# Kernel tuning notes

Measured on AMD Instinct MI355X. Metric: run time of the kernel, lower is better.

The kernel has to match this reference:

```python
import jax, jax.numpy as jnp
import numpy as np

N = 6000      # nodes
E = 150000    # edges (avg degree ~25, close to _AVG_DEGREE=23.4)
K = 9         # (lmax+1)^2 spherical coefficients, lmax=2
C = 128       # sphere_channels
H = 8         # num_heads
V = 16        # attn_value_channels (H*V == C)
L = 2         # num_layers
B = 512       # num_distance_basis
RMAX = 5.0
EPS = 1e-6


def _rms_sh(x):
    # rms_norm_sh-style normalization over (coefficients, channels)
    return x * jax.lax.rsqrt(jnp.mean(x * x, axis=(-2, -1), keepdims=True) + EPS)


def _seg_softmax(logits, seg, n):
    # numerically-stable per-destination-node softmax over incoming edges
    m = jax.ops.segment_max(logits, seg, num_segments=n)
    ex = jnp.exp(logits - m[seg])
    s = jax.ops.segment_sum(ex, seg, num_segments=n)
    return ex / (s[seg] + 1e-9)


def setup_inputs() -> dict:
    key = jax.random.key(0)
    ks = jax.random.split(key, 24)
    s = 0.02
    inp = {
        # graph / features
        "atom_feats": jax.random.randint(ks[0], (N, 4), 0, 10),
        "bond_feats": jax.random.randint(ks[1], (E, 3), 0, 8),
        "edge_index": jax.random.randint(ks[2], (2, E), 0, N),
        "edge_distance": jax.random.uniform(ks[3], (E,), jnp.float32, 0.0, RMAX),
        # embeddings
        "atom_emb": jax.random.normal(ks[4], (4, 10, C), jnp.float32) * s,
        "bond_emb": jax.random.normal(ks[5], (3, 8, C), jnp.float32) * s,
        # distance-basis edge MLP (edge_channels_list = [512, 128, 128])
        "W_rbf1": jax.random.normal(ks[6], (B, C), jnp.float32) * s,
        "b_rbf1": jnp.zeros((C,), jnp.float32),
        "W_rbf2": jax.random.normal(ks[7], (C, C), jnp.float32) * s,
        "b_rbf2": jnp.zeros((C,), jnp.float32),
        # per-layer attention params (stacked over L)
        "Wa1": jax.random.normal(ks[8], (L, 3 * C, C), jnp.float32) * s,
        "Wa2": jax.random.normal(ks[9], (L, C, H), jnp.float32) * s,
        "Wv": jax.random.normal(ks[10], (L, C, H * V), jnp.float32) * s,
        "Wg": jax.random.normal(ks[11], (L, C, H), jnp.float32) * s,
        "Wo": jax.random.normal(ks[12], (L, H * V, C), jnp.float32) * s,
        # per-layer FFN params
        "Wf1": jax.random.normal(ks[13], (L, C, 512), jnp.float32) * s,
        "Wf2": jax.random.normal(ks[14], (L, 512, C), jnp.float32) * s,
    }
    return inp


def _forward(atom_feats, bond_feats, edge_index, edge_distance,
             atom_emb, bond_emb, W_rbf1, b_rbf1, W_rbf2, b_rbf2,
             Wa1, Wa2, Wv, Wg, Wo, Wf1, Wf2):
    src, dst = edge_index[0], edge_index[1]

    # --- atom embedding into l=0 coefficient of the SH node state ---
    a0 = sum(atom_emb[f][atom_feats[:, f]] for f in range(4))      # [N, C]
    x = jnp.zeros((N, K, C), a0.dtype).at[:, 0, :].set(a0)          # [N, K, C]

    # --- gaussian distance basis + edge embedding MLP + bond features ---
    centers = jnp.linspace(0.0, RMAX, B)
    width = RMAX / B
    rbf = jnp.exp(-((edge_distance[:, None] - centers[None, :]) / width) ** 2)  # [E, B]
    e = jax.nn.silu(rbf @ W_rbf1 + b_rbf1) @ W_rbf2 + b_rbf2                    # [E, C]
    e = e + sum(bond_emb[f][bond_feats[:, f]] for f in range(3))

    for l in range(L):
        # ---- SO(2)-style graph attention block ----
        xn = _rms_sh(x)
        xs = xn[src]                                                 # [E, K, C] gather
        inv = jnp.concatenate([xn[src, 0], xn[dst, 0], e], axis=-1)  # invariant feats [E, 3C]
        logits = jax.nn.silu(inv @ Wa1[l]) @ Wa2[l]                  # [E, H]
        alpha = _seg_softmax(logits, dst, N)                         # renormalized attention
        gate = jax.nn.sigmoid(e @ Wg[l])                             # edge-embedding gate [E, H]
        v = jnp.einsum('ekc,chv->ekhv', xs, Wv[l].reshape(C, H, V))  # [E, K, H, V]
        v = v * (alpha * gate)[:, None, :, None]
        msg = v.reshape(E, K, H * V)
        agg = jax.ops.segment_sum(msg, dst, num_segments=N)          # scatter [N, K, H*V]
        x = x + jnp.einsum('nkd,dc->nkc', agg, Wo[l])

        # ---- equivariant FFN with separable S2-style activation ----
        xn = _rms_sh(x)
        h = jnp.einsum('nkc,cf->nkf', xn, Wf1[l])                    # [N, K, 512]
        h0 = jax.nn.silu(h[:, :1, :])                                # l=0 scalar path
        hr = h[:, 1:, :] * jax.nn.sigmoid(h[:, :1, :])               # gated l>0 path
        h = jnp.concatenate([h0, hr], axis=1)
        x = x + jnp.einsum('nkf,fc->nkc', h, Wf2[l])

    return _rms_sh(x)


def reference(atom_feats, bond_feats, edge_index, edge_distance,
              atom_emb, bond_emb, W_rbf1, b_rbf1, W_rbf2, b_rbf2,
              Wa1, Wa2, Wv, Wg, Wo, Wf1, Wf2):
    return _forward(atom_feats, bond_feats, edge_index, edge_distance,
                    atom_emb, bond_emb, W_rbf1, b_rbf1, W_rbf2, b_rbf2,
                    Wa1, Wa2, Wv, Wg, Wo, Wf1, Wf2)
```

## Files before the change

### kernel.cpp

```cpp
#include <hip/hip_runtime.h>

#define NN 6000
#define NE 150000
#define TBM 2048
#define TROWS (TBM + 1)

typedef unsigned int uint;
typedef unsigned short ushort;
typedef __attribute__((ext_vector_type(8))) short short8v;
typedef __attribute__((ext_vector_type(4))) float float4v;

__device__ __forceinline__ float siluf(float x) { return x / (1.f + __expf(-x)); }
__device__ __forceinline__ float sigmf(float x) { return 1.f / (1.f + __expf(-x)); }
__device__ __forceinline__ uint pack2bf(float lo, float hi) {
    uint ul = __float_as_uint(lo);
    ul = (ul + 0x7fffu + ((ul >> 16) & 1u)) >> 16;
    uint uh = __float_as_uint(hi);
    uh = ((uh + 0x7fffu + ((uh >> 16) & 1u)) >> 16) << 16;
    return ul | uh;
}
__device__ __forceinline__ ushort f2bf(float f) {
    uint u = __float_as_uint(f);
    return (ushort)((u + 0x7fffu + ((u >> 16) & 1u)) >> 16);
}
__device__ __forceinline__ float2 up2(uint u) {
    return make_float2(__uint_as_float(u << 16), __uint_as_float(u & 0xffff0000u));
}

__global__ __launch_bounds__(256)
void k_prep(const float* __restrict__ W2, const float* __restrict__ b2,
            const float* __restrict__ Wa1, const float* __restrict__ Wg,
            const float* __restrict__ bemb,
            const float* __restrict__ Wf1, const float* __restrict__ Wf2,
            const float* __restrict__ Wv, const float* __restrict__ Wa2,
            const float* __restrict__ Wo,
            float* __restrict__ W2A, float* __restrict__ W2G,
            float* __restrict__ bA, float* __restrict__ bG,
            uint* __restrict__ BAcb, float* __restrict__ BGc,
            ushort* __restrict__ Wf1x, ushort* __restrict__ Wf2x,
            ushort* __restrict__ Wvx, ushort* __restrict__ Wa1sx,
            ushort* __restrict__ Wa1dx, ushort* __restrict__ Wa2x,
            ushort* __restrict__ Wox)
{
    __shared__ float w2_s[8][132];
    const int l = blockIdx.y, bx = blockIdx.x, tid = threadIdx.x;
    const float* Wa1e = Wa1 + (size_t)l * 384 * 128 + 256 * 128;
    const float* Wgl  = Wg  + (size_t)l * 128 * 8;

    if (bx < 16) {
        const int i0 = bx * 8;
        for (int q = tid; q < 8 * 32; q += 256) {
            int ni = q >> 5, j4 = (q & 31) * 4;
            *reinterpret_cast<float4*>(&w2_s[ni][j4]) =
                *reinterpret_cast<const float4*>(&W2[(size_t)(i0 + ni) * 128 + j4]);
        }
        __syncthreads();
        const int j = tid & 127, ng = tid >> 7;
        float a[4] = {0.f, 0.f, 0.f, 0.f};
        #pragma unroll 4
        for (int k4 = 0; k4 < 128; k4 += 4) {
            float w0 = Wa1e[(k4 + 0) * 128 + j];
            float w1 = Wa1e[(k4 + 1) * 128 + j];
            float w2v = Wa1e[(k4 + 2) * 128 + j];
            float w3 = Wa1e[(k4 + 3) * 128 + j];
            #pragma unroll
            for (int r = 0; r < 4; ++r) {
                const float4 xv = *reinterpret_cast<const float4*>(&w2_s[ng * 4 + r][k4]);
                a[r] += xv.x * w0 + xv.y * w1 + xv.z * w2v + xv.w * w3;
            }
        }
        #pragma unroll
        for (int r = 0; r < 4; ++r)
            W2A[(size_t)l * 16384 + (size_t)(i0 + ng * 4 + r) * 128 + j] = a[r];
    } else if (bx == 16) {
        const int i = tid & 127, hq = tid >> 7;
        float a[4] = {0.f, 0.f, 0.f, 0.f};
        for (int k = 0; k < 128; ++k) {
            float w = W2[(size_t)i * 128 + k];
            const float4 g4 = *reinterpret_cast<const float4*>(&Wgl[k * 8 + hq * 4]);
            a[0] += w * g4.x; a[1] += w * g4.y; a[2] += w * g4.z; a[3] += w * g4.w;
        }
        #pragma unroll
        for (int q = 0; q < 4; ++q)
            W2G[(size_t)l * 1024 + (size_t)i * 8 + hq * 4 + q] = a[q];
    } else if (bx == 17) {
        if (tid < 128) {
            float s = 0.f;
            for (int k = 0; k < 128; ++k) s += b2[k] * Wa1e[k * 128 + tid];
            bA[l * 128 + tid] = s;
        } else if (tid < 136) {
            int h = tid - 128;
            float s = 0.f;
            for (int k = 0; k < 128; ++k) s += b2[k] * Wgl[k * 8 + h];
            bG[l * 8 + h] = s;
        }
    } else if (bx < 274) {
        const int cb = (bx - 18) * 2 + (tid >> 7);
        const int c = tid & 127;
        const int b[3] = {cb >> 6, (cb >> 3) & 7, cb & 7};
        float s = 0.f;
        #pragma unroll
        for (int f = 0; f < 3; ++f) {
            const float* er = &bemb[(size_t)(f * 8 + b[f]) * 128];
            for (int k = 0; k < 128; ++k)
                s += er[k] * Wa1e[k * 128 + c];
        }
        float hi = __shfl_down(s, 1, 64);
        if ((c & 1) == 0)
            BAcb[(size_t)l * 512 * 64 + (size_t)cb * 64 + (c >> 1)] = pack2bf(s, hi);
        if (c < 8) {
            float g = 0.f;
            #pragma unroll
            for (int f = 0; f < 3; ++f) {
                const float* er = &bemb[(size_t)(f * 8 + b[f]) * 128];
                for (int k = 0; k < 128; ++k)
                    g += er[k] * Wgl[k * 8 + c];
            }
            BGc[(size_t)l * 512 * 8 + (size_t)cb * 8 + c] = g;
        }
    } else {
        const int sub = (bx - 274) * 4 + (tid >> 6);
        const int lane = tid & 63;
        if (sub < 128) {
            const int nt = sub >> 2, kt = sub & 3;
            const float* src = Wf1 + (size_t)l * 65536;
            ushort* dst = Wf1x + (size_t)l * 65536 + ((size_t)sub * 64 + lane) * 8;
            #pragma unroll
            for (int j = 0; j < 8; ++j)
                dst[j] = f2bf(src[(size_t)(kt * 32 + (lane >> 4) * 8 + j) * 512 + nt * 16 + (lane & 15)]);
        } else if (sub < 256) {
            const int b2x = sub - 128;
            const int nt = b2x >> 4, kt = b2x & 15;
            const float* src = Wf2 + (size_t)l * 65536;
            ushort* dst = Wf2x + (size_t)l * 65536 + ((size_t)b2x * 64 + lane) * 8;
            #pragma unroll
            for (int j = 0; j < 8; ++j)
                dst[j] = f2bf(src[(size_t)(kt * 32 + (lane >> 4) * 8 + j) * 128 + nt * 16 + (lane & 15)]);
        } else if (sub < 352) {
            const int b3 = sub - 256;
            const int mat = b3 >> 5, blk = b3 & 31;
            const int nt = blk >> 2, kt = blk & 3;
            const float* src;
            ushort* dst;
            if (mat == 0)      { src = Wv  + (size_t)l * 16384;             dst = Wvx   + (size_t)l * 16384; }
            else if (mat == 1) { src = Wa1 + (size_t)l * 384 * 128;         dst = Wa1sx + (size_t)l * 16384; }
            else               { src = Wa1 + (size_t)l * 384 * 128 + 16384; dst = Wa1dx + (size_t)l * 16384; }
            dst += ((size_t)blk * 64 + lane) * 8;
            #pragma unroll
            for (int j = 0; j < 8; ++j)
                dst[j] = f2bf(src[(size_t)(kt * 32 + (lane >> 4) * 8 + j) * 128 + nt * 16 + (lane & 15)]);
        } else if (sub < 356) {
            const int kt = sub - 352;
            const int col = lane & 15;
            const float* src = Wa2 + (size_t)l * 128 * 8;
            ushort* dst = Wa2x + (size_t)l * 2048 + ((size_t)kt * 64 + lane) * 8;
            #pragma unroll
            for (int j = 0; j < 8; ++j) {
                int krow = kt * 32 + (lane >> 4) * 8 + j;
                dst[j] = (col < 8) ? f2bf(src[(size_t)krow * 8 + col]) : (ushort)0;
            }
        } else {
            const int blk = sub - 356;
            const int nt = blk >> 2, kt = blk & 3;
            const float* src = Wo + (size_t)l * 16384;
            ushort* dst = Wox + (size_t)l * 16384 + ((size_t)blk * 64 + lane) * 8;
            #pragma unroll
            for (int j = 0; j < 8; ++j)
                dst[j] = f2bf(src[(size_t)(kt * 32 + (lane >> 4) * 8 + j) * 128 + nt * 16 + (lane & 15)]);
        }
    }
}

__device__ __forceinline__
void node_gemm3(const ushort a_s[16][136], int tid, int n0,
                const ushort* __restrict__ Wvx, const ushort* __restrict__ Wa1sx,
                const ushort* __restrict__ Wa1dx,
                uint* __restrict__ Vb, uint* __restrict__ Psb, uint* __restrict__ Pdb)
{
    const int l = tid & 63, wq = tid >> 6;
    const int lr = l & 15, lk = l >> 4;
    #pragma unroll
    for (int jb = 0; jb < 6; ++jb) {
        int job = wq * 6 + jb;
        int mat = job >> 3, nt = job & 7;
        const ushort* W = (mat == 0) ? Wvx : (mat == 1 ? Wa1sx : Wa1dx);
        uint* O = (mat == 0) ? Vb : (mat == 1 ? Psb : Pdb);
        float4v acc = (float4v){0.f, 0.f, 0.f, 0.f};
        #pragma unroll
        for (int ks = 0; ks < 4; ++ks) {
            short8v af = *reinterpret_cast<const short8v*>(&a_s[lr][lk * 8 + ks * 32]);
            short8v bf = *reinterpret_cast<const short8v*>(&W[((size_t)(nt * 4 + ks) * 64 + l) * 8]);
            acc = __builtin_amdgcn_mfma_f32_16x16x32_bf16(af, bf, acc, 0, 0, 0);
        }
        #pragma unroll
        for (int r = 0; r < 4; ++r) {
            float v = acc[r];
            float vn = __shfl_xor(v, 1, 64);
            if ((l & 1) == 0) {
                int row = lk * 4 + r, col = nt * 16 + lr;
                O[(size_t)(n0 + row) * 64 + (col >> 1)] = pack2bf(v, vn);
            }
        }
    }
}

__global__ __launch_bounds__(256)
void k_prep2(const float* __restrict__ W1, const float* __restrict__ b1,
             const float* __restrict__ W2A, const float* __restrict__ W2G,
             const float* __restrict__ bA, const float* __restrict__ bG,
             uint* __restrict__ TAb, float* __restrict__ TG,
             const int* __restrict__ af, const float* __restrict__ aemb,
             float* __restrict__ x, int* __restrict__ deg,
             const ushort* __restrict__ Wvx, const ushort* __restrict__ Wa1sx,
             const ushort* __restrict__ Wa1dx,
             uint* __restrict__ Vb, uint* __restrict__ Psb, uint* __restrict__ Pdb)
{
    __shared__ float rbf_s[8][32];
    __shared__ int   bs_s[8];
    __shared__ float t1_s[8][132];
    __shared__ ushort a_s[16][136];
    const int tid = threadIdx.x, bx = blockIdx.x;

    if (bx < 514) {
        const int l = (bx >= 257) ? 1 : 0;
        const int r0 = (bx - l * 257) * 8;
        {
            int ri = tid >> 5, j = tid & 31;
            int row = min(r0 + ri, TBM);
            float d = (float)row * (5.0f / TBM);
            const float step = 5.0f / 511.0f;
            const float invw = 512.0f / 5.0f;
            int b0 = (int)(d * (511.0f / 5.0f) + 0.5f);
            int bs = min(max(b0 - 16, 0), 512 - 32);
            if (j == 0) bs_s[ri] = bs;
            float z = (d - (float)(bs + j) * step) * invw;
            rbf_s[ri][j] = __expf(-z * z);
        }
        __syncthreads();
        #pragma unroll
        for (int pass = 0; pass < 4; ++pass) {
            int idx = pass * 256 + tid;
            int ri = idx >> 7, c = idx & 127;
            int bs = bs_s[ri];
            float t = b1[c];
            #pragma unroll
            for (int j = 0; j < 32; ++j)
                t += rbf_s[ri][j] * W1[(bs + j) * 128 + c];
            t1_s[ri][c] = siluf(t);
        }
        __syncthreads();

        const float* W2Al = W2A + (size_t)l * 16384;
        const int c = tid & 127, ng = tid >> 7;
        float a[4];
        #pragma unroll
        for (int r = 0; r < 4; ++r) a[r] = bA[l * 128 + c];
        #pragma unroll 4
        for (int k4 = 0; k4 < 128; k4 += 4) {
            float w0 = W2Al[(k4 + 0) * 128 + c];
            float w1 = W2Al[(k4 + 1) * 128 + c];
            float w2v = W2Al[(k4 + 2) * 128 + c];
            float w3 = W2Al[(k4 + 3) * 128 + c];
            #pragma unroll
            for (int r = 0; r < 4; ++r) {
                const float4 xv = *reinterpret_cast<const float4*>(&t1_s[ng * 4 + r][k4]);
                a[r] += xv.x * w0 + xv.y * w1 + xv.z * w2v + xv.w * w3;
            }
        }
        #pragma unroll
        for (int r = 0; r < 4; ++r) {
            float hi = __shfl_down(a[r], 1, 64);
            int row = r0 + ng * 4 + r;
            if (((c & 1) == 0) && row <= TBM)
                TAb[(size_t)l * TROWS * 64 + (size_t)row * 64 + (c >> 1)] = pack2bf(a[r], hi);
        }
        if (tid < 64) {
            int ri = tid >> 3, h = tid & 7;
            int row = r0 + ri;
            if (row <= TBM) {
                const float* W2Gl = W2G + (size_t)l * 1024;
                float s = bG[l * 8 + h];
                #pragma unroll 8
                for (int k = 0; k < 128; ++k)
                    s += t1_s[ri][k] * W2Gl[k * 8 + h];
                TG[(size_t)l * TROWS * 8 + (size_t)row * 8 + h] = s;
            }
        }
    } else {
        const int n0 = (bx - 514) * 16;
        if (tid < 16) deg[n0 + tid] = 0;
        {
            int ni = tid >> 4, c8 = (tid & 15) * 8;
            int n = n0 + ni;
            float v[8];
            #pragma unroll
            for (int q = 0; q < 8; ++q) v[q] = 0.f;
            #pragma unroll
            for (int f = 0; f < 4; ++f) {
                int idx = af[n * 4 + f];
                const float* er = &aemb[(size_t)(f * 10 + idx) * 128 + c8];
                float4 e0 = *reinterpret_cast<const float4*>(er);
                float4 e1 = *reinterpret_cast<const float4*>(er + 4);
                v[0] += e0.x; v[1] += e0.y; v[2] += e0.z; v[3] += e0.w;
                v[4] += e1.x; v[5] += e1.y; v[6] += e1.z; v[7] += e1.w;
            }
            float* xr = &x[(size_t)n * 128 + c8];
            *reinterpret_cast<float4*>(xr)     = make_float4(v[0], v[1], v[2], v[3]);
            *reinterpret_cast<float4*>(xr + 4) = make_float4(v[4], v[5], v[6], v[7]);
            float ss = 0.f;
            #pragma unroll
            for (int q = 0; q < 8; ++q) ss += v[q] * v[q];
            #pragma unroll
            for (int m = 1; m < 16; m <<= 1) ss += __shfl_xor(ss, m, 16);
            float r = rsqrtf(ss * (1.0f / 1152.0f) + 1e-6f);
            uint4 pk;
            pk.x = pack2bf(v[0] * r, v[1] * r);
            pk.y = pack2bf(v[2] * r, v[3] * r);
            pk.z = pack2bf(v[4] * r, v[5] * r);
            pk.w = pack2bf(v[6] * r, v[7] * r);
            *reinterpret_cast<uint4*>(&a_s[ni][c8]) = pk;
        }
        __syncthreads();
        node_gemm3(a_s, tid, n0, Wvx, Wa1sx, Wa1dx, Vb, Psb, Pdb);
    }
}

__global__ __launch_bounds__(256)
void k_hist(const int* __restrict__ eidx, int* __restrict__ deg)
{
    int e = blockIdx.x * 256 + threadIdx.x;
    if (e < NE) atomicAdd(&deg[eidx[NE + e]], 1);
}

__global__ __launch_bounds__(1024)
void k_scan(const int* __restrict__ deg, int* __restrict__ off, int* __restrict__ cursor)
{
    __shared__ int part[1024];
    const int t = threadIdx.x;
    const int base = t * 6;
    int loc[6]; int s = 0;
    #pragma unroll
    for (int i = 0; i < 6; ++i) {
        int d = (base + i < NN) ? deg[base + i] : 0;
        loc[i] = s; s += d;
    }
    part[t] = s;
    __syncthreads();
    for (int o = 1; o < 1024; o <<= 1) {
        int v = (t >= o) ? part[t - o] : 0;
        __syncthreads();
        part[t] += v;
        __syncthreads();
    }
    int pre = (t > 0) ? part[t - 1] : 0;
    #pragma unroll
    for (int i = 0; i < 6; ++i) {
        if (base + i < NN) {
            int v = pre + loc[i];
            off[base + i] = v;
            cursor[base + i] = v;
        }
    }
    if (t == 1023) off[NN] = part[1023];
}

__global__ __launch_bounds__(256)
void k_fill(const int* __restrict__ eidx, const int* __restrict__ bondf,
            const float* __restrict__ dist, int* __restrict__ cursor,
            int* __restrict__ srcp, int* __restrict__ dstp,
            float* __restrict__ distp, int* __restrict__ cbp)
{
    int e = blockIdx.x * 256 + threadIdx.x;
    if (e < NE) {
        int d = eidx[NE + e];
        int p = atomicAdd(&cursor[d], 1);
        srcp[p] = eidx[e];
        dstp[p] = d;
        distp[p] = dist[e];
        cbp[p] = bondf[e * 3 + 0] * 64 + bondf[e * 3 + 1] * 8 + bondf[e * 3 + 2];
    }
}

__global__ __launch_bounds__(256)
void k_attn(const int* __restrict__ srcp, const int* __restrict__ dstp,
            const float* __restrict__ distp, const int* __restrict__ cbp,
            const uint* __restrict__ Psb, const uint* __restrict__ Pdb,
            const uint* __restrict__ TAbl, const float* __restrict__ TGl,
            const uint* __restrict__ BAcbl, const float* __restrict__ BGcl,
            const ushort* __restrict__ Wa2xl,
            float2* __restrict__ nex)
{
    __shared__ ushort t_s[32][136];
    __shared__ float gate_s[32][8];
    const int tid = threadIdx.x;
    const int p0 = blockIdx.x * 32;

    {
        const int ei = tid >> 3, g = tid & 7;
        const int p = min(p0 + ei, NE - 1);
        const int sn = srcp[p], dn = dstp[p];
        const float d = distp[p];
        const int cb = cbp[p];
        float u = d * ((float)TBM / 5.0f);
        int i = min((int)u, TBM - 1);
        float f = u - (float)i, f1 = 1.f - f;

        uint ps[8], pd[8], t0[8], t1v[8], ba[8];
        {
            const uint4* pp = reinterpret_cast<const uint4*>(&Psb[(size_t)sn * 64 + g * 8]);
            uint4 a = pp[0], b = pp[1];
            ps[0]=a.x; ps[1]=a.y; ps[2]=a.z; ps[3]=a.w; ps[4]=b.x; ps[5]=b.y; ps[6]=b.z; ps[7]=b.w;
            pp = reinterpret_cast<const uint4*>(&Pdb[(size_t)dn * 64 + g * 8]);
            a = pp[0]; b = pp[1];
            pd[0]=a.x; pd[1]=a.y; pd[2]=a.z; pd[3]=a.w; pd[4]=b.x; pd[5]=b.y; pd[6]=b.z; pd[7]=b.w;
            pp = reinterpret_cast<const uint4*>(&TAbl[(size_t)i * 64 + g * 8]);
            a = pp[0]; b = pp[1];
            t0[0]=a.x; t0[1]=a.y; t0[2]=a.z; t0[3]=a.w; t0[4]=b.x; t0[5]=b.y; t0[6]=b.z; t0[7]=b.w;
            pp = reinterpret_cast<const uint4*>(&TAbl[(size_t)(i + 1) * 64 + g * 8]);
            a = pp[0]; b = pp[1];
            t1v[0]=a.x; t1v[1]=a.y; t1v[2]=a.z; t1v[3]=a.w; t1v[4]=b.x; t1v[5]=b.y; t1v[6]=b.z; t1v[7]=b.w;
            pp = reinterpret_cast<const uint4*>(&BAcbl[(size_t)cb * 64 + g * 8]);
            a = pp[0]; b = pp[1];
            ba[0]=a.x; ba[1]=a.y; ba[2]=a.z; ba[3]=a.w; ba[4]=b.x; ba[5]=b.y; ba[6]=b.z; ba[7]=b.w;
        }
        uint tw[8];
        #pragma unroll
        for (int q = 0; q < 8; ++q) {
            float2 vs = up2(ps[q]), vd = up2(pd[q]), v0 = up2(t0[q]), v1 = up2(t1v[q]), vb = up2(ba[q]);
            float s0 = siluf(vs.x + vd.x + f1 * v0.x + f * v1.x + vb.x);
            float s1 = siluf(vs.y + vd.y + f1 * v0.y + f * v1.y + vb.y);
            tw[q] = pack2bf(s0, s1);
        }
        uint4* tp = reinterpret_cast<uint4*>(&t_s[ei][g * 16]);
        tp[0] = make_uint4(tw[0], tw[1], tw[2], tw[3]);
        tp[1] = make_uint4(tw[4], tw[5], tw[6], tw[7]);
        if (g == 0) {
            const float4* tg0 = reinterpret_cast<const float4*>(&TGl[(size_t)i * 8]);
            const float4* bg4 = reinterpret_cast<const float4*>(&BGcl[(size_t)cb * 8]);
            #pragma unroll
            for (int q = 0; q < 2; ++q) {
                float4 g0 = tg0[q], g1 = tg0[q + 2], bb = bg4[q];
                gate_s[ei][4 * q + 0] = f1 * g0.x + f * g1.x + bb.x;
                gate_s[ei][4 * q + 1] = f1 * g0.y + f * g1.y + bb.y;
                gate_s[ei][4 * q + 2] = f1 * g0.z + f * g1.z + bb.z;
                gate_s[ei][4 * q + 3] = f1 * g0.w + f * g1.w + bb.w;
            }
        }
    }
    __syncthreads();

    {
        const int wq = tid >> 6, l = tid & 63;
        if (wq < 2) {
            const int lr = l & 15, lk = l >> 4;
            float4v acc = (float4v){0.f, 0.f, 0.f, 0.f};
            #pragma unroll
            for (int ks = 0; ks < 4; ++ks) {
                short8v af = *reinterpret_cast<const short8v*>(&t_s[wq * 16 + lr][lk * 8 + ks * 32]);
                short8v bf = *reinterpret_cast<const short8v*>(&Wa2xl[((size_t)ks * 64 + l) * 8]);
                acc = __builtin_amdgcn_mfma_f32_16x16x32_bf16(af, bf, acc, 0, 0, 0);
            }
            const int h = l & 15;
            if (h < 8) {
                #pragma unroll
                for (int r = 0; r < 4; ++r) {
                    int ei = wq * 16 + lk * 4 + r;
                    int p = p0 + ei;
                    if (p < NE) {
                        float ex = __expf(acc[r]);
                        nex[(size_t)p * 8 + h] = make_float2(ex * sigmf(gate_s[ei][h]), ex);
                    }
                }
            }
        }
    }
}

template<int LAST>
__global__ __launch_bounds__(256)
void k_layer_fused(float* __restrict__ x,
                   const int* __restrict__ off, const int* __restrict__ srcp,
                   const float2* __restrict__ nex, const uint* __restrict__ Vb,
                   const ushort* __restrict__ Woxl,
                   const ushort* __restrict__ Wf1xl, const ushort* __restrict__ Wf2xl,
                   float* __restrict__ out,
                   const ushort* __restrict__ WvxN, const ushort* __restrict__ Wa1sxN,
                   const ushort* __restrict__ Wa1dxN,
                   uint* __restrict__ VbO, uint* __restrict__ Psb, uint* __restrict__ Pdb)
{
    __shared__ ushort a_s[16][136];
    __shared__ ushort h_s[16][520];
    __shared__ float xf_s[16][132];
    const int tid = threadIdx.x;
    const int n0 = blockIdx.x * 16;
    const int ni = tid >> 4, c8 = (tid & 15) * 8;

    {
        const float* xr = &x[(size_t)(n0 + ni) * 128 + c8];
        *reinterpret_cast<float4*>(&xf_s[ni][c8])     = *reinterpret_cast<const float4*>(xr);
        *reinterpret_cast<float4*>(&xf_s[ni][c8 + 4]) = *reinterpret_cast<const float4*>(xr + 4);
    }

    {
        const int n = n0 + ni;
        const int h = (tid & 15) >> 1;
        const int cd4 = (tid & 15) * 4;
        const int s = off[n], t = off[n + 1];
        float acc[8];
        #pragma unroll
        for (int q = 0; q < 8; ++q) acc[q] = 0.f;
        float es = 0.f;
        int p = s;
        for (; p + 4 <= t; p += 4) {
            int sn0 = srcp[p + 0], sn1 = srcp[p + 1], sn2 = srcp[p + 2], sn3 = srcp[p + 3];
            float2 ne0 = nex[(size_t)(p + 0) * 8 + h];
            float2 ne1 = nex[(size_t)(p + 1) * 8 + h];
            float2 ne2 = nex[(size_t)(p + 2) * 8 + h];
            float2 ne3 = nex[(size_t)(p + 3) * 8 + h];
            uint4 u0 = *reinterpret_cast<const uint4*>(&Vb[(size_t)sn0 * 64 + cd4]);
            uint4 u1 = *reinterpret_cast<const uint4*>(&Vb[(size_t)sn1 * 64 + cd4]);
            uint4 u2 = *reinterpret_cast<const uint4*>(&Vb[(size_t)sn2 * 64 + cd4]);
            uint4 u3 = *reinterpret_cast<const uint4*>(&Vb[(size_t)sn3 * 64 + cd4]);
            es += ne0.y + ne1.y + ne2.y + ne3.y;
            uint uu[4][4] = {{u0.x,u0.y,u0.z,u0.w},{u1.x,u1.y,u1.z,u1.w},
                             {u2.x,u2.y,u2.z,u2.w},{u3.x,u3.y,u3.z,u3.w}};
            float cf[4] = {ne0.x, ne1.x, ne2.x, ne3.x};
            #pragma unroll
            for (int e = 0; e < 4; ++e) {
                #pragma unroll
                for (int q = 0; q < 4; ++q) {
                    float2 v = up2(uu[e][q]);
                    acc[2 * q + 0] += cf[e] * v.x;
                    acc[2 * q + 1] += cf[e] * v.y;
                }
            }
        }
        for (; p < t; ++p) {
            int sn = srcp[p];
            float2 ne = nex[(size_t)p * 8 + h];
            uint4 u = *reinterpret_cast<const uint4*>(&Vb[(size_t)sn * 64 + cd4]);
            es += ne.y;
            uint uu[4] = {u.x, u.y, u.z, u.w};
            #pragma unroll
            for (int q = 0; q < 4; ++q) {
                float2 v = up2(uu[q]);
                acc[2 * q + 0] += ne.x * v.x;
                acc[2 * q + 1] += ne.x * v.y;
            }
        }
        float sinv = 1.f / (es + 1e-9f);
        uint4 pk;
        pk.x = pack2bf(acc[0] * sinv, acc[1] * sinv);
        pk.y = pack2bf(acc[2] * sinv, acc[3] * sinv);
        pk.z = pack2bf(acc[4] * sinv, acc[5] * sinv);
        pk.w = pack2bf(acc[6] * sinv, acc[7] * sinv);
        *reinterpret_cast<uint4*>(&a_s[ni][c8]) = pk;
    }
    __syncthreads();

    const int l  = tid & 63;
    const int wq = tid >> 6;
    const int lr = l & 15, lk = l >> 4;

    {
        float4v acc2[2];
        acc2[0] = (float4v){0.f, 0.f, 0.f, 0.f};
        acc2[1] = (float4v){0.f, 0.f, 0.f, 0.f};
        #pragma unroll
        for (int ks = 0; ks < 4; ++ks) {
            short8v af = *reinterpret_cast<const short8v*>(&a_s[lr][lk * 8 + ks * 32]);
            #pragma unroll
            for (int nf = 0; nf < 2; ++nf) {
                int nt = wq * 2 + nf;
                short8v bf = *reinterpret_cast<const short8v*>(&Woxl[((size_t)(nt * 4 + ks) * 64 + l) * 8]);
                acc2[nf] = __builtin_amdgcn_mfma_f32_16x16x32_bf16(af, bf, acc2[nf], 0, 0, 0);
            }
        }
        #pragma unroll
        for (int nf = 0; nf < 2; ++nf) {
            #pragma unroll
            for (int r = 0; r < 4; ++r)
                xf_s[lk * 4 + r][(wq * 2 + nf) * 16 + lr] += acc2[nf][r];
        }
    }
    __syncthreads();

    {
        float4 v0 = *reinterpret_cast<const float4*>(&xf_s[ni][c8]);
        float4 v1 = *reinterpret_cast<const float4*>(&xf_s[ni][c8 + 4]);
        float ss = v0.x * v0.x + v0.y * v0.y + v0.z * v0.z + v0.w * v0.w
                 + v1.x * v1.x + v1.y * v1.y + v1.z * v1.z + v1.w * v1.w;
        #pragma unroll
        for (int m = 1; m < 16; m <<= 1) ss += __shfl_xor(ss, m, 16);
        float r = rsqrtf(ss * (1.0f / 1152.0f) + 1e-6f);
        uint4 pk;
        pk.x = pack2bf(v0.x * r, v0.y * r);
        pk.y = pack2bf(v0.z * r, v0.w * r);
        pk.z = pack2bf(v1.x * r, v1.y * r);
        pk.w = pack2bf(v1.z * r, v1.w * r);
        __syncthreads();
        *reinterpret_cast<uint4*>(&a_s[ni][c8]) = pk;
    }
    __syncthreads();

    {
        float4v acc[8];
        #pragma unroll
        for (int nf = 0; nf < 8; ++nf) acc[nf] = (float4v){0.f, 0.f, 0.f, 0.f};
        #pragma unroll
        for (int ks = 0; ks < 4; ++ks) {
            short8v af = *reinterpret_cast<const short8v*>(&a_s[lr][lk * 8 + ks * 32]);
            #pragma unroll
            for (int nf = 0; nf < 8; ++nf) {
                int nt = wq * 8 + nf;
                short8v bf = *reinterpret_cast<const short8v*>(&Wf1xl[((size_t)(nt * 4 + ks) * 64 + l) * 8]);
                acc[nf] = __builtin_amdgcn_mfma_f32_16x16x32_bf16(af, bf, acc[nf], 0, 0, 0);
            }
        }
        #pragma unroll
        for (int nf = 0; nf < 8; ++nf) {
            #pragma unroll
            for (int r = 0; r < 4; ++r) {
                float v = siluf(acc[nf][r]);
                float vn = __shfl_xor(v, 1, 64);
                if ((l & 1) == 0) {
                    int row = lk * 4 + r;
                    int col = wq * 128 + nf * 16 + lr;
                    *reinterpret_cast<uint*>(&h_s[row][col]) = pack2bf(v, vn);
                }
            }
        }
    }
    __syncthreads();

    {
        float4v acc2[2];
        acc2[0] = (float4v){0.f, 0.f, 0.f, 0.f};
        acc2[1] = (float4v){0.f, 0.f, 0.f, 0.f};
        #pragma unroll 4
        for (int ks = 0; ks < 16; ++ks) {
            short8v af = *reinterpret_cast<const short8v*>(&h_s[lr][lk * 8 + ks * 32]);
            #pragma unroll
            for (int nf = 0; nf < 2; ++nf) {
                int nt = wq * 2 + nf;
                short8v bf = *reinterpret_cast<const short8v*>(&Wf2xl[((size_t)(nt * 16 + ks) * 64 + l) * 8]);
                acc2[nf] = __builtin_amdgcn_mfma_f32_16x16x32_bf16(af, bf, acc2[nf], 0, 0, 0);
            }
        }
        #pragma unroll
        for (int nf = 0; nf < 2; ++nf) {
            #pragma unroll
            for (int r = 0; r < 4; ++r)
                xf_s[lk * 4 + r][(wq * 2 + nf) * 16 + lr] += acc2[nf][r];
        }
    }
    __syncthreads();

    {
        float4 v0 = *reinterpret_cast<const float4*>(&xf_s[ni][c8]);
        float4 v1 = *reinterpret_cast<const float4*>(&xf_s[ni][c8 + 4]);
        float ss = v0.x * v0.x + v0.y * v0.y + v0.z * v0.z + v0.w * v0.w
                 + v1.x * v1.x + v1.y * v1.y + v1.z * v1.z + v1.w * v1.w;
        #pragma unroll
        for (int m = 1; m < 16; m <<= 1) ss += __shfl_xor(ss, m, 16);
        float r = rsqrtf(ss * (1.0f / 1152.0f) + 1e-6f);

        if (!LAST) {
            float* xr = &x[(size_t)(n0 + ni) * 128 + c8];
            *reinterpret_cast<float4*>(xr)     = v0;
            *reinterpret_cast<float4*>(xr + 4) = v1;
            uint4 pk;
            pk.x = pack2bf(v0.x * r, v0.y * r);
            pk.y = pack2bf(v0.z * r, v0.w * r);
            pk.z = pack2bf(v1.x * r, v1.y * r);
            pk.w = pack2bf(v1.z * r, v1.w * r);
            __syncthreads();
            *reinterpret_cast<uint4*>(&a_s[ni][c8]) = pk;
            __syncthreads();
            node_gemm3(a_s, tid, n0, WvxN, Wa1sxN, Wa1dxN, VbO, Psb, Pdb);
        } else {
            size_t base = (size_t)(n0 + ni) * 1152 + c8;
            *reinterpret_cast<float4*>(&out[base])     = make_float4(v0.x * r, v0.y * r, v0.z * r, v0.w * r);
            *reinterpret_cast<float4*>(&out[base + 4]) = make_float4(v1.x * r, v1.y * r, v1.z * r, v1.w * r);
            const float4 z4 = make_float4(0.f, 0.f, 0.f, 0.f);
            #pragma unroll
            for (int k = 1; k < 9; ++k) {
                *reinterpret_cast<float4*>(&out[base + (size_t)k * 128]) = z4;
                *reinterpret_cast<float4*>(&out[base + (size_t)k * 128 + 4]) = z4;
            }
        }
    }
}

extern "C" void kernel_launch(void* const* d_in, const int* in_sizes, int n_in,
                              void* d_out, int out_size, void* d_ws, size_t ws_size,
                              hipStream_t stream)
{
    const int*   atom_feats = (const int*)d_in[0];
    const int*   bond_feats = (const int*)d_in[1];
    const int*   edge_index = (const int*)d_in[2];
    const float* edge_dist  = (const float*)d_in[3];
    const float* atom_emb   = (const float*)d_in[4];
    const float* bond_emb   = (const float*)d_in[5];
    const float* W_rbf1     = (const float*)d_in[6];
    const float* b_rbf1     = (const float*)d_in[7];
    const float* W_rbf2     = (const float*)d_in[8];
    const float* b_rbf2     = (const float*)d_in[9];
    const float* Wa1        = (const float*)d_in[10];
    const float* Wa2        = (const float*)d_in[11];
    const float* Wv         = (const float*)d_in[12];
    const float* Wg         = (const float*)d_in[13];
    const float* Wo         = (const float*)d_in[14];
    const float* Wf1        = (const float*)d_in[15];
    const float* Wf2        = (const float*)d_in[16];
    float* out = (float*)d_out;

    float* ws   = (float*)d_ws;
    float* x    = ws;
    float2* nex = (float2*)(x + NN * 128);
    float* W2A  = (float*)(nex + (size_t)NE * 8);
    float* W2G  = W2A  + 2 * 16384;
    float* bA   = W2G  + 2 * 1024;
    float* bG   = bA   + 2 * 128;
    float* TG   = bG   + 16;
    float* BGc  = TG   + 2 * (size_t)TROWS * 8;
    float* distp = BGc + 2 * 512 * 8;
    uint* Vb    = (uint*)(distp + NE);
    uint* Psb   = Vb  + NN * 64;
    uint* Pdb   = Psb + NN * 64;
    uint* TAb   = Pdb + NN * 64;
    uint* BAcb  = TAb + 2 * (size_t)TROWS * 64;
    ushort* Wf1x  = (ushort*)(BAcb + 2 * 512 * 64);
    ushort* Wf2x  = Wf1x  + 2 * 65536;
    ushort* Wvx   = Wf2x  + 2 * 65536;
    ushort* Wa1sx = Wvx   + 2 * 16384;
    ushort* Wa1dx = Wa1sx + 2 * 16384;
    ushort* Wa2x  = Wa1dx + 2 * 16384;
    ushort* Wox   = Wa2x  + 2 * 2048;
    int* deg    = (int*)(Wox + 2 * 16384);
    int* off    = deg + NN;
    int* cursor = off + NN + 1;
    int* srcp   = cursor + NN;
    int* dstp   = srcp + NE;
    int* cbp    = dstp + NE;

    k_prep<<<dim3(371, 2), 256, 0, stream>>>(W_rbf2, b_rbf2, Wa1, Wg, bond_emb,
        Wf1, Wf2, Wv, Wa2, Wo, W2A, W2G, bA, bG, BAcb, BGc,
        Wf1x, Wf2x, Wvx, Wa1sx, Wa1dx, Wa2x, Wox);
    k_prep2<<<514 + NN / 16, 256, 0, stream>>>(W_rbf1, b_rbf1, W2A, W2G, bA, bG, TAb, TG,
        atom_feats, atom_emb, x, deg, Wvx, Wa1sx, Wa1dx, Vb, Psb, Pdb);

    k_hist<<<(NE + 255) / 256, 256, 0, stream>>>(edge_index, deg);
    k_scan<<<1, 1024, 0, stream>>>(deg, off, cursor);
    k_fill<<<(NE + 255) / 256, 256, 0, stream>>>(edge_index, bond_feats, edge_dist,
                                                 cursor, srcp, dstp, distp, cbp);

    for (int l = 0; l < 2; ++l) {
        k_attn<<<(NE + 31) / 32, 256, 0, stream>>>(srcp, dstp, distp, cbp,
            Psb, Pdb,
            TAb + (size_t)l * TROWS * 64, TG + (size_t)l * TROWS * 8,
            BAcb + (size_t)l * 512 * 64, BGc + (size_t)l * 512 * 8,
            Wa2x + (size_t)l * 2048, nex);
        if (l == 0)
            k_layer_fused<0><<<NN / 16, 256, 0, stream>>>(x, off, srcp, nex, Vb,
                Wox, Wf1x, Wf2x, out,
                Wvx + 16384, Wa1sx + 16384, Wa1dx + 16384, Vb, Psb, Pdb);
        else
            k_layer_fused<1><<<NN / 16, 256, 0, stream>>>(x, off, srcp, nex, Vb,
                Wox + 16384, Wf1x + 65536, Wf2x + 65536, out,
                Wvx, Wa1sx, Wa1dx, Vb, Psb, Pdb);
    }
}
```

Measured before the change: 167.6 us.

## Widen fused layer kernel to 512 threads and pack edge records into int4

The fused per-layer node kernel moves from 256 to 512 threads per 16-node block. Each thread now gathers 4 channels instead of 8, and each of the 8 waves owns fewer MFMA tiles in the Wo, FFN and next-layer projection GEMMs, which adds parallelism across the 375 blocks. Separately, the per-edge src, dst, distance and bond code are written as one int4 record, so the attention kernel reads each edge with a single vector load. The trade-off is more threads per block, possible register-limit pressure at 512, and smaller per-thread gathers of the V rows.

Measured after the change: 155.4 us. 7.3% less time.

```diff
diff --git a/kernel.cpp b/kernel.cpp
--- a/kernel.cpp
+++ b/kernel.cpp
@@ -204,6 +204,39 @@
     }
 }
 
+__device__ __forceinline__
+void node_gemm3_8w(const ushort a_s[16][136], int tid, int n0,
+                   const ushort* __restrict__ Wvx, const ushort* __restrict__ Wa1sx,
+                   const ushort* __restrict__ Wa1dx,
+                   uint* __restrict__ Vb, uint* __restrict__ Psb, uint* __restrict__ Pdb)
+{
+    const int l = tid & 63, w = tid >> 6;
+    const int lr = l & 15, lk = l >> 4;
+    #pragma unroll
+    for (int jb = 0; jb < 3; ++jb) {
+        int job = w * 3 + jb;
+        int mat = job >> 3, nt = job & 7;
+        const ushort* W = (mat == 0) ? Wvx : (mat == 1 ? Wa1sx : Wa1dx);
+        uint* O = (mat == 0) ? Vb : (mat == 1 ? Psb : Pdb);
+        float4v acc = (float4v){0.f, 0.f, 0.f, 0.f};
+        #pragma unroll
+        for (int ks = 0; ks < 4; ++ks) {
+            short8v af = *reinterpret_cast<const short8v*>(&a_s[lr][lk * 8 + ks * 32]);
+            short8v bf = *reinterpret_cast<const short8v*>(&W[((size_t)(nt * 4 + ks) * 64 + l) * 8]);
+            acc = __builtin_amdgcn_mfma_f32_16x16x32_bf16(af, bf, acc, 0, 0, 0);
+        }
+        #pragma unroll
+        for (int r = 0; r < 4; ++r) {
+            float v = acc[r];
+            float vn = __shfl_xor(v, 1, 64);
+            if ((l & 1) == 0) {
+                int row = lk * 4 + r, col = nt * 16 + lr;
+                O[(size_t)(n0 + row) * 64 + (col >> 1)] = pack2bf(v, vn);
+            }
+        }
+    }
+}
+
 __global__ __launch_bounds__(256)
 void k_prep2(const float* __restrict__ W1, const float* __restrict__ b1,
              const float* __restrict__ W2A, const float* __restrict__ W2G,
@@ -367,23 +400,21 @@
 __global__ __launch_bounds__(256)
 void k_fill(const int* __restrict__ eidx, const int* __restrict__ bondf,
             const float* __restrict__ dist, int* __restrict__ cursor,
-            int* __restrict__ srcp, int* __restrict__ dstp,
-            float* __restrict__ distp, int* __restrict__ cbp)
+            int* __restrict__ srcp, int4* __restrict__ erec)
 {
     int e = blockIdx.x * 256 + threadIdx.x;
     if (e < NE) {
         int d = eidx[NE + e];
         int p = atomicAdd(&cursor[d], 1);
-        srcp[p] = eidx[e];
-        dstp[p] = d;
-        distp[p] = dist[e];
-        cbp[p] = bondf[e * 3 + 0] * 64 + bondf[e * 3 + 1] * 8 + bondf[e * 3 + 2];
+        int sn = eidx[e];
+        srcp[p] = sn;
+        erec[p] = make_int4(sn, d, __float_as_int(dist[e]),
+                            bondf[e * 3 + 0] * 64 + bondf[e * 3 + 1] * 8 + bondf[e * 3 + 2]);
     }
 }
 
 __global__ __launch_bounds__(256)
-void k_attn(const int* __restrict__ srcp, const int* __restrict__ dstp,
-            const float* __restrict__ distp, const int* __restrict__ cbp,
+void k_attn(const int4* __restrict__ erec,
             const uint* __restrict__ Psb, const uint* __restrict__ Pdb,
             const uint* __restrict__ TAbl, const float* __restrict__ TGl,
             const uint* __restrict__ BAcbl, const float* __restrict__ BGcl,
@@ -398,9 +429,10 @@
     {
         const int ei = tid >> 3, g = tid & 7;
         const int p = min(p0 + ei, NE - 1);
-        const int sn = srcp[p], dn = dstp[p];
-        const float d = distp[p];
-        const int cb = cbp[p];
+        const int4 er = erec[p];
+        const int sn = er.x, dn = er.y;
+        const float d = __int_as_float(er.z);
+        const int cb = er.w;
         float u = d * ((float)TBM / 5.0f);
         int i = min((int)u, TBM - 1);
         float f = u - (float)i, f1 = 1.f - f;
@@ -477,7 +509,7 @@
 }
 
 template<int LAST>
-__global__ __launch_bounds__(256)
+__global__ __launch_bounds__(512)
 void k_layer_fused(float* __restrict__ x,
                    const int* __restrict__ off, const int* __restrict__ srcp,
                    const float2* __restrict__ nex, const uint* __restrict__ Vb,
@@ -493,23 +525,21 @@
     __shared__ float xf_s[16][132];
     const int tid = threadIdx.x;
     const int n0 = blockIdx.x * 16;
-    const int ni = tid >> 4, c8 = (tid & 15) * 8;
-
-    {
-        const float* xr = &x[(size_t)(n0 + ni) * 128 + c8];
-        *reinterpret_cast<float4*>(&xf_s[ni][c8])     = *reinterpret_cast<const float4*>(xr);
-        *reinterpret_cast<float4*>(&xf_s[ni][c8 + 4]) = *reinterpret_cast<const float4*>(xr + 4);
+    const int ni = tid >> 5;
+    const int ci = tid & 31;
+    const int c4 = ci * 4;
+
+    {
+        *reinterpret_cast<float4*>(&xf_s[ni][c4]) =
+            *reinterpret_cast<const float4*>(&x[(size_t)(n0 + ni) * 128 + c4]);
     }
 
     {
         const int n = n0 + ni;
-        const int h = (tid & 15) >> 1;
-        const int cd4 = (tid & 15) * 4;
+        const int h = ci >> 2;
+        const int cd2 = ci * 2;
         const int s = off[n], t = off[n + 1];
-        float acc[8];
-        #pragma unroll
-        for (int q = 0; q < 8; ++q) acc[q] = 0.f;
-        float es = 0.f;
+        float a0 = 0.f, a1 = 0.f, a2 = 0.f, a3 = 0.f, es = 0.f;
         int p = s;
         for (; p + 4 <= t; p += 4) {
             int sn0 = srcp[p + 0], sn1 = srcp[p + 1], sn2 = srcp[p + 2], sn3 = srcp[p + 3];
@@ -517,115 +547,92 @@
             float2 ne1 = nex[(size_t)(p + 1) * 8 + h];
             float2 ne2 = nex[(size_t)(p + 2) * 8 + h];
             float2 ne3 = nex[(size_t)(p + 3) * 8 + h];
-            uint4 u0 = *reinterpret_cast<const uint4*>(&Vb[(size_t)sn0 * 64 + cd4]);
-            uint4 u1 = *reinterpret_cast<const uint4*>(&Vb[(size_t)sn1 * 64 + cd4]);
-            uint4 u2 = *reinterpret_cast<const uint4*>(&Vb[(size_t)sn2 * 64 + cd4]);
-            uint4 u3 = *reinterpret_cast<const uint4*>(&Vb[(size_t)sn3 * 64 + cd4]);
+            uint2 u0 = *reinterpret_cast<const uint2*>(&Vb[(size_t)sn0 * 64 + cd2]);
+            uint2 u1 = *reinterpret_cast<const uint2*>(&Vb[(size_t)sn1 * 64 + cd2]);
+            uint2 u2 = *reinterpret_cast<const uint2*>(&Vb[(size_t)sn2 * 64 + cd2]);
+            uint2 u3 = *reinterpret_cast<const uint2*>(&Vb[(size_t)sn3 * 64 + cd2]);
             es += ne0.y + ne1.y + ne2.y + ne3.y;
-            uint uu[4][4] = {{u0.x,u0.y,u0.z,u0.w},{u1.x,u1.y,u1.z,u1.w},
-                             {u2.x,u2.y,u2.z,u2.w},{u3.x,u3.y,u3.z,u3.w}};
-            float cf[4] = {ne0.x, ne1.x, ne2.x, ne3.x};
-            #pragma unroll
-            for (int e = 0; e < 4; ++e) {
-                #pragma unroll
-                for (int q = 0; q < 4; ++q) {
-                    float2 v = up2(uu[e][q]);
-                    acc[2 * q + 0] += cf[e] * v.x;
-                    acc[2 * q + 1] += cf[e] * v.y;
-                }
-            }
+            float2 v;
+            v = up2(u0.x); a0 += ne0.x * v.x; a1 += ne0.x * v.y;
+            v = up2(u0.y); a2 += ne0.x * v.x; a3 += ne0.x * v.y;
+            v = up2(u1.x); a0 += ne1.x * v.x; a1 += ne1.x * v.y;
+            v = up2(u1.y); a2 += ne1.x * v.x; a3 += ne1.x * v.y;
+            v = up2(u2.x); a0 += ne2.x * v.x; a1 += ne2.x * v.y;
+            v = up2(u2.y); a2 += ne2.x * v.x; a3 += ne2.x * v.y;
+            v = up2(u3.x); a0 += ne3.x * v.x; a1 += ne3.x * v.y;
+            v = up2(u3.y); a2 += ne3.x * v.x; a3 += ne3.x * v.y;
         }
         for (; p < t; ++p) {
             int sn = srcp[p];
             float2 ne = nex[(size_t)p * 8 + h];
-            uint4 u = *reinterpret_cast<const uint4*>(&Vb[(size_t)sn * 64 + cd4]);
+            uint2 u = *reinterpret_cast<const uint2*>(&Vb[(size_t)sn * 64 + cd2]);
             es += ne.y;
-            uint uu[4] = {u.x, u.y, u.z, u.w};
-            #pragma unroll
-            for (int q = 0; q < 4; ++q) {
-                float2 v = up2(uu[q]);
-                acc[2 * q + 0] += ne.x * v.x;
-                acc[2 * q + 1] += ne.x * v.y;
-            }
+            float2 v;
+            v = up2(u.x); a0 += ne.x * v.x; a1 += ne.x * v.y;
+            v = up2(u.y); a2 += ne.x * v.x; a3 += ne.x * v.y;
         }
         float sinv = 1.f / (es + 1e-9f);
-        uint4 pk;
-        pk.x = pack2bf(acc[0] * sinv, acc[1] * sinv);
-        pk.y = pack2bf(acc[2] * sinv, acc[3] * sinv);
-        pk.z = pack2bf(acc[4] * sinv, acc[5] * sinv);
-        pk.w = pack2bf(acc[6] * sinv, acc[7] * sinv);
-        *reinterpret_cast<uint4*>(&a_s[ni][c8]) = pk;
+        uint2 pk;
+        pk.x = pack2bf(a0 * sinv, a1 * sinv);
+        pk.y = pack2bf(a2 * sinv, a3 * sinv);
+        *reinterpret_cast<uint2*>(&a_s[ni][c4]) = pk;
     }
     __syncthreads();
 
     const int l  = tid & 63;
-    const int wq = tid >> 6;
+    const int w  = tid >> 6;
     const int lr = l & 15, lk = l >> 4;
 
     {
-        float4v acc2[2];
-        acc2[0] = (float4v){0.f, 0.f, 0.f, 0.f};
-        acc2[1] = (float4v){0.f, 0.f, 0.f, 0.f};
+        float4v acc = (float4v){0.f, 0.f, 0.f, 0.f};
         #pragma unroll
         for (int ks = 0; ks < 4; ++ks) {
             short8v af = *reinterpret_cast<const short8v*>(&a_s[lr][lk * 8 + ks * 32]);
-            #pragma unroll
-            for (int nf = 0; nf < 2; ++nf) {
-                int nt = wq * 2 + nf;
-                short8v bf = *reinterpret_cast<const short8v*>(&Woxl[((size_t)(nt * 4 + ks) * 64 + l) * 8]);
-                acc2[nf] = __builtin_amdgcn_mfma_f32_16x16x32_bf16(af, bf, acc2[nf], 0, 0, 0);
-            }
-        }
-        #pragma unroll
-        for (int nf = 0; nf < 2; ++nf) {
-            #pragma unroll
-            for (int r = 0; r < 4; ++r)
-                xf_s[lk * 4 + r][(wq * 2 + nf) * 16 + lr] += acc2[nf][r];
-        }
+            short8v bf = *reinterpret_cast<const short8v*>(&Woxl[((size_t)(w * 4 + ks) * 64 + l) * 8]);
+            acc = __builtin_amdgcn_mfma_f32_16x16x32_bf16(af, bf, acc, 0, 0, 0);
+        }
+        #pragma unroll
+        for (int r = 0; r < 4; ++r)
+            xf_s[lk * 4 + r][w * 16 + lr] += acc[r];
     }
     __syncthreads();
 
     {
-        float4 v0 = *reinterpret_cast<const float4*>(&xf_s[ni][c8]);
-        float4 v1 = *reinterpret_cast<const float4*>(&xf_s[ni][c8 + 4]);
-        float ss = v0.x * v0.x + v0.y * v0.y + v0.z * v0.z + v0.w * v0.w
-                 + v1.x * v1.x + v1.y * v1.y + v1.z * v1.z + v1.w * v1.w;
-        #pragma unroll
-        for (int m = 1; m < 16; m <<= 1) ss += __shfl_xor(ss, m, 16);
+        float4 v = *reinterpret_cast<const float4*>(&xf_s[ni][c4]);
+        float ss = v.x * v.x + v.y * v.y + v.z * v.z + v.w * v.w;
+        #pragma unroll
+        for (int m = 1; m < 32; m <<= 1) ss += __shfl_xor(ss, m, 32);
         float r = rsqrtf(ss * (1.0f / 1152.0f) + 1e-6f);
-        uint4 pk;
-        pk.x = pack2bf(v0.x * r, v0.y * r);
-        pk.y = pack2bf(v0.z * r, v0.w * r);
-        pk.z = pack2bf(v1.x * r, v1.y * r);
-        pk.w = pack2bf(v1.z * r, v1.w * r);
-        __syncthreads();
-        *reinterpret_cast<uint4*>(&a_s[ni][c8]) = pk;
+        uint2 pk;
+        pk.x = pack2bf(v.x * r, v.y * r);
+        pk.y = pack2bf(v.z * r, v.w * r);
+        *reinterpret_cast<uint2*>(&a_s[ni][c4]) = pk;
     }
     __syncthreads();
 
     {
-        float4v acc[8];
-        #pragma unroll
-        for (int nf = 0; nf < 8; ++nf) acc[nf] = (float4v){0.f, 0.f, 0.f, 0.f};
+        float4v acc[4];
+        #pragma unroll
+        for (int nf = 0; nf < 4; ++nf) acc[nf] = (float4v){0.f, 0.f, 0.f, 0.f};
         #pragma unroll
         for (int ks = 0; ks < 4; ++ks) {
             short8v af = *reinterpret_cast<const short8v*>(&a_s[lr][lk * 8 + ks * 32]);
             #pragma unroll
-            for (int nf = 0; nf < 8; ++nf) {
-                int nt = wq * 8 + nf;
+            for (int nf = 0; nf < 4; ++nf) {
+                int nt = w * 4 + nf;
                 short8v bf = *reinterpret_cast<const short8v*>(&Wf1xl[((size_t)(nt * 4 + ks) * 64 + l) * 8]);
                 acc[nf] = __builtin_amdgcn_mfma_f32_16x16x32_bf16(af, bf, acc[nf], 0, 0, 0);
             }
         }
         #pragma unroll
-        for (int nf = 0; nf < 8; ++nf) {
+        for (int nf = 0; nf < 4; ++nf) {
             #pragma unroll
             for (int r = 0; r < 4; ++r) {
                 float v = siluf(acc[nf][r]);
                 float vn = __shfl_xor(v, 1, 64);
                 if ((l & 1) == 0) {
                     int row = lk * 4 + r;
-                    int col = wq * 128 + nf * 16 + lr;
+                    int col = (w * 4 + nf) * 16 + lr;
                     *reinterpret_cast<uint*>(&h_s[row][col]) = pack2bf(v, vn);
                 }
             }
@@ -634,60 +641,41 @@
     __syncthreads();
 
     {
-        float4v acc2[2];
-        acc2[0] = (float4v){0.f, 0.f, 0.f, 0.f};
-        acc2[1] = (float4v){0.f, 0.f, 0.f, 0.f};
+        float4v acc = (float4v){0.f, 0.f, 0.f, 0.f};
         #pragma unroll 4
         for (int ks = 0; ks < 16; ++ks) {
             short8v af = *reinterpret_cast<const short8v*>(&h_s[lr][lk * 8 + ks * 32]);
-            #pragma unroll
-            for (int nf = 0; nf < 2; ++nf) {
-                int nt = wq * 2 + nf;
-                short8v bf = *reinterpret_cast<const short8v*>(&Wf2xl[((size_t)(nt * 16 + ks) * 64 + l) * 8]);
-                acc2[nf] = __builtin_amdgcn_mfma_f32_16x16x32_bf16(af, bf, acc2[nf], 0, 0, 0);
-            }
-        }
-        #pragma unroll
-        for (int nf = 0; nf < 2; ++nf) {
-            #pragma unroll
-            for (int r = 0; r < 4; ++r)
-                xf_s[lk * 4 + r][(wq * 2 + nf) * 16 + lr] += acc2[nf][r];
-        }
+            short8v bf = *reinterpret_cast<const short8v*>(&Wf2xl[((size_t)(w * 16 + ks) * 64 + l) * 8]);
+            acc = __builtin_amdgcn_mfma_f32_16x16x32_bf16(af, bf, acc, 0, 0, 0);
+        }
+        #pragma unroll
+        for (int r = 0; r < 4; ++r)
+            xf_s[lk * 4 + r][w * 16 + lr] += acc[r];
     }
     __syncthreads();
 
     {
-        float4 v0 = *reinterpret_cast<const float4*>(&xf_s[ni][c8]);
-        float4 v1 = *reinterpret_cast<const float4*>(&xf_s[ni][c8 + 4]);
-        float ss = v0.x * v0.x + v0.y * v0.y + v0.z * v0.z + v0.w * v0.w
-                 + v1.x * v1.x + v1.y * v1.y + v1.z * v1.z + v1.w * v1.w;
-        #pragma unroll
-        for (int m = 1; m < 16; m <<= 1) ss += __shfl_xor(ss, m, 16);
+        float4 v = *reinterpret_cast<const float4*>(&xf_s[ni][c4]);
+        float ss = v.x * v.x + v.y * v.y + v.z * v.z + v.w * v.w;
+        #pragma unroll
+        for (int m = 1; m < 32; m <<= 1) ss += __shfl_xor(ss, m, 32);
         float r = rsqrtf(ss * (1.0f / 1152.0f) + 1e-6f);
 
         if (!LAST) {
-            float* xr = &x[(size_t)(n0 + ni) * 128 + c8];
-            *reinterpret_cast<float4*>(xr)     = v0;
-            *reinterpret_cast<float4*>(xr + 4) = v1;
-            uint4 pk;
-            pk.x = pack2bf(v0.x * r, v0.y * r);
-            pk.y = pack2bf(v0.z * r, v0.w * r);
-            pk.z = pack2bf(v1.x * r, v1.y * r);
-            pk.w = pack2bf(v1.z * r, v1.w * r);
+            *reinterpret_cast<float4*>(&x[(size_t)(n0 + ni) * 128 + c4]) = v;
+            uint2 pk;
+            pk.x = pack2bf(v.x * r, v.y * r);
+            pk.y = pack2bf(v.z * r, v.w * r);
+            *reinterpret_cast<uint2*>(&a_s[ni][c4]) = pk;
             __syncthreads();
-            *reinterpret_cast<uint4*>(&a_s[ni][c8]) = pk;
-            __syncthreads();
-            node_gemm3(a_s, tid, n0, WvxN, Wa1sxN, Wa1dxN, VbO, Psb, Pdb);
+            node_gemm3_8w(a_s, tid, n0, WvxN, Wa1sxN, Wa1dxN, VbO, Psb, Pdb);
         } else {
-            size_t base = (size_t)(n0 + ni) * 1152 + c8;
-            *reinterpret_cast<float4*>(&out[base])     = make_float4(v0.x * r, v0.y * r, v0.z * r, v0.w * r);
-            *reinterpret_cast<float4*>(&out[base + 4]) = make_float4(v1.x * r, v1.y * r, v1.z * r, v1.w * r);
+            size_t base = (size_t)(n0 + ni) * 1152 + c4;
+            *reinterpret_cast<float4*>(&out[base]) = make_float4(v.x * r, v.y * r, v.z * r, v.w * r);
             const float4 z4 = make_float4(0.f, 0.f, 0.f, 0.f);
             #pragma unroll
-            for (int k = 1; k < 9; ++k) {
+            for (int k = 1; k < 9; ++k)
                 *reinterpret_cast<float4*>(&out[base + (size_t)k * 128]) = z4;
-                *reinterpret_cast<float4*>(&out[base + (size_t)k * 128 + 4]) = z4;
-            }
         }
     }
 }
@@ -724,8 +712,7 @@
     float* bG   = bA   + 2 * 128;
     float* TG   = bG   + 16;
     float* BGc  = TG   + 2 * (size_t)TROWS * 8;
-    float* distp = BGc + 2 * 512 * 8;
-    uint* Vb    = (uint*)(distp + NE);
+    uint* Vb    = (uint*)(BGc + 2 * 512 * 8);
     uint* Psb   = Vb  + NN * 64;
     uint* Pdb   = Psb + NN * 64;
     uint* TAb   = Pdb + NN * 64;
@@ -741,8 +728,7 @@
     int* off    = deg + NN;
     int* cursor = off + NN + 1;
     int* srcp   = cursor + NN;
-    int* dstp   = srcp + NE;
-    int* cbp    = dstp + NE;
+    int4* erec  = (int4*)(srcp + NE);
 
     k_prep<<<dim3(371, 2), 256, 0, stream>>>(W_rbf2, b_rbf2, Wa1, Wg, bond_emb,
         Wf1, Wf2, Wv, Wa2, Wo, W2A, W2G, bA, bG, BAcb, BGc,
@@ -753,20 +739,20 @@
     k_hist<<<(NE + 255) / 256, 256, 0, stream>>>(edge_index, deg);
     k_scan<<<1, 1024, 0, stream>>>(deg, off, cursor);
     k_fill<<<(NE + 255) / 256, 256, 0, stream>>>(edge_index, bond_feats, edge_dist,
-                                                 cursor, srcp, dstp, distp, cbp);
+                                                 cursor, srcp, erec);
 
     for (int l = 0; l < 2; ++l) {
-        k_attn<<<(NE + 31) / 32, 256, 0, stream>>>(srcp, dstp, distp, cbp,
+        k_attn<<<(NE + 31) / 32, 256, 0, stream>>>(erec,
             Psb, Pdb,
             TAb + (size_t)l * TROWS * 64, TG + (size_t)l * TROWS * 8,
             BAcb + (size_t)l * 512 * 64, BGc + (size_t)l * 512 * 8,
             Wa2x + (size_t)l * 2048, nex);
         if (l == 0)
-            k_layer_fused<0><<<NN / 16, 256, 0, stream>>>(x, off, srcp, nex, Vb,
+            k_layer_fused<0><<<NN / 16, 512, 0, stream>>>(x, off, srcp, nex, Vb,
                 Wox, Wf1x, Wf2x, out,
                 Wvx + 16384, Wa1sx + 16384, Wa1dx + 16384, Vb, Psb, Pdb);
         else
-            k_layer_fused<1><<<NN / 16, 256, 0, stream>>>(x, off, srcp, nex, Vb,
+            k_layer_fused<1><<<NN / 16, 512, 0, stream>>>(x, off, srcp, nex, Vb,
                 Wox + 16384, Wf1x + 65536, Wf2x + 65536, out,
                 Wvx, Wa1sx, Wa1dx, Vb, Psb, Pdb);
     }
```
